# Optimization experiments

Hardware: AMD Instinct MI355X
Metric: run time of the kernel (lower is better)

## Reference

```python
import jax, jax.numpy as jnp
import numpy as np

EPS = 1e-12  # matches torch F.normalize default eps


def setup_inputs() -> dict:
    key = jax.random.key(0)
    img_feats = jax.random.normal(key, (8192, 1024), dtype=jnp.float32)
    return {"img_feats": img_feats}


def reference(img_feats):
    # L2-normalize along feature dim (torch F.normalize: x / max(||x||, eps))
    norm = jnp.maximum(jnp.linalg.norm(img_feats, axis=-1, keepdims=True), EPS)
    feats_n = img_feats / norm                       # [N, D]
    sims = feats_n @ feats_n.T                        # [N, N] cosine similarities
    # mask self-similarity on the diagonal with -inf
    n = sims.shape[0]
    diag = jnp.arange(n)
    sims = sims.at[diag, diag].set(-jnp.inf)
    attn_weights = jax.nn.softmax(sims, axis=-1)      # [N, N]
    out = attn_weights @ img_feats                    # [N, D]
    return out, attn_weights
```

## Files before the change

kernel.cpp:

```cpp
#include <hip/hip_runtime.h>
#include <hip/hip_bf16.h>
#include <stdint.h>

#define NR 8192
#define ND 1024

typedef __attribute__((ext_vector_type(8))) short bf16x8;
typedef __attribute__((ext_vector_type(4))) float f32x4;
typedef __attribute__((ext_vector_type(4))) float fvec4;
typedef __attribute__((ext_vector_type(8))) unsigned short u16x8;

static __device__ __forceinline__ uint16_t f2bf(float f) {
  union { __hip_bfloat16 h; uint16_t u; } cv;
  cv.h = __float2bfloat16(f);
  return cv.u;
}
static __device__ __forceinline__ float bf2f(uint16_t u) {
  union { uint32_t i; float f; } cv;
  cv.i = ((uint32_t)u) << 16;
  return cv.f;
}

__global__ void k_norm(const float* __restrict__ X, uint16_t* __restrict__ Xn) {
  const int row = blockIdx.x;
  const int t = threadIdx.x;
  const float4 v = reinterpret_cast<const float4*>(X + (size_t)row * ND)[t];
  float ss = v.x * v.x + v.y * v.y + v.z * v.z + v.w * v.w;
#pragma unroll
  for (int m = 1; m < 64; m <<= 1) ss += __shfl_xor(ss, m, 64);
  __shared__ float sred[4];
  if ((t & 63) == 0) sred[t >> 6] = ss;
  __syncthreads();
  const float tot = sred[0] + sred[1] + sred[2] + sred[3];
  const float inv = 1.0f / fmaxf(sqrtf(tot), 1e-12f);
  ushort4 o;
  o.x = f2bf(v.x * inv); o.y = f2bf(v.y * inv);
  o.z = f2bf(v.z * inv); o.w = f2bf(v.w * inv);
  reinterpret_cast<ushort4*>(Xn + (size_t)row * ND)[t] = o;
}

__global__ void k_transpose(const float* __restrict__ X, uint16_t* __restrict__ XT) {
  __shared__ uint16_t tile[32][33];
  const int ntr = NR / 32;
  const int bx = blockIdx.x % ntr;
  const int by = blockIdx.x / ntr;
  const int r0 = bx * 32, d0 = by * 32;
  const int t = threadIdx.x;
  const int rr = t >> 3, cc = (t & 7) * 4;
  const float4 v = *reinterpret_cast<const float4*>(&X[(size_t)(r0 + rr) * ND + d0 + cc]);
  tile[cc + 0][rr] = f2bf(v.x);
  tile[cc + 1][rr] = f2bf(v.y);
  tile[cc + 2][rr] = f2bf(v.z);
  tile[cc + 3][rr] = f2bf(v.w);
  __syncthreads();
  ushort4 o;
  o.x = tile[rr][cc + 0]; o.y = tile[rr][cc + 1];
  o.z = tile[rr][cc + 2]; o.w = tile[rr][cc + 3];
  *reinterpret_cast<ushort4*>(&XT[(size_t)(d0 + rr) * NR + r0 + cc]) = o;
}

template <int HALF>
static __device__ __forceinline__ void mfma32(f32x4 (&acc)[8][4],
                                              const bf16x8 (&a_)[4][2],
                                              const bf16x8 (&b_)[4][2]) {
  __builtin_amdgcn_s_setprio(1);
#pragma unroll
  for (int kk = 0; kk < 2; ++kk)
#pragma unroll
    for (int m4 = 0; m4 < 4; ++m4)
#pragma unroll
      for (int n = 0; n < 4; ++n)
        acc[HALF * 4 + m4][n] = __builtin_amdgcn_mfma_f32_16x16x32_bf16(
            a_[m4][kk], b_[n][kk], acc[HALF * 4 + m4][n], 0, 0, 0);
  __builtin_amdgcn_s_setprio(0);
}

#define BAR()    __builtin_amdgcn_s_barrier()
#define LGKM()   asm volatile("s_waitcnt lgkmcnt(0)" ::: "memory")
#define VMW8()   asm volatile("s_waitcnt vmcnt(8)" ::: "memory")
#define VMW0()   asm volatile("s_waitcnt vmcnt(0)" ::: "memory")
#define SCHED0() __builtin_amdgcn_sched_barrier(0)

template <int EPI, int NKT>
static __device__ __forceinline__ void gemm8_core(
    char* sm,
    const uint16_t* __restrict__ A, int lda,
    const uint16_t* __restrict__ B, int ldb,
    int row0, int col0,
    float* __restrict__ C, int ldc,
    uint16_t* __restrict__ Eo, float* __restrict__ partials, int rb, int cb) {
  const int tid = threadIdx.x;
  const int wid = tid >> 6;
  const int lane = tid & 63;
  const int wr = wid >> 2;
  const int wc = wid & 3;
  const int flane = lane & 15;
  const int qw = lane >> 4;
  const int rkey = flane & 7;
  const int rowb = flane * 128;

  const int colb = (((tid & 7) ^ ((tid >> 3) & 7)) * 16);
  const int r0s = tid >> 3;

  const char* const Abyte = (const char*)A + (size_t)row0 * lda * 2;
  const char* const Bbyte = (const char*)B + (size_t)col0 * ldb * 2;

  f32x4 acc[8][4] = {};
  bf16x8 a_[4][2], b_[4][2];

  auto stage = [&](int d, int isB, int h, int t) {
    const char* gb = isB ? Bbyte : Abyte;
    const int ld2 = (isB ? ldb : lda) * 2;
    const char* g0 = gb + (size_t)(h * 128 + r0s) * ld2 + t * 128 + colb;
    const char* g1 = g0 + (size_t)64 * ld2;
    char* l0 = sm + d * 65536 + isB * 32768 + h * 16384 + (wid << 10);
    __builtin_amdgcn_global_load_lds((const __attribute__((address_space(1))) void*)g0,
                                     (__attribute__((address_space(3))) void*)l0, 16, 0, 0);
    __builtin_amdgcn_global_load_lds((const __attribute__((address_space(1))) void*)g1,
                                     (__attribute__((address_space(3))) void*)(l0 + 8192), 16, 0, 0);
  };
  auto stage4 = [&](int d, int t) {
    stage(d, 0, 0, t); stage(d, 0, 1, t); stage(d, 1, 0, t); stage(d, 1, 1, t);
  };
  auto rdA = [&](int d, int mhalf) {
#pragma unroll
    for (int m4 = 0; m4 < 4; ++m4)
#pragma unroll
      for (int kk = 0; kk < 2; ++kk) {
        const int chunk = (qw + kk * 4) ^ rkey;
        a_[m4][kk] = *(const bf16x8*)(sm + d * 65536 + wr * 16384 +
                                      (mhalf * 4 + m4) * 2048 + rowb + chunk * 16);
      }
  };
  auto rdB = [&](int d) {
#pragma unroll
    for (int n = 0; n < 4; ++n)
#pragma unroll
      for (int kk = 0; kk < 2; ++kk) {
        const int chunk = (qw + kk * 4) ^ rkey;
        b_[n][kk] = *(const bf16x8*)(sm + d * 65536 + 32768 + (wc >> 1) * 16384 +
                                     (wc & 1) * 8192 + n * 2048 + rowb + chunk * 16);
      }
  };

  auto ktile = [&](int d) {
    rdB(d); rdA(d, 0);
    LGKM(); SCHED0();
    mfma32<0>(acc, a_, b_);
    rdA(d, 1);
    LGKM(); SCHED0();
    mfma32<1>(acc, a_, b_);
  };

  stage4(0, 0);
  stage4(1, 1);
  VMW8();
  BAR();

  const int niter = NKT / 2;
  for (int i = 0; i < niter; ++i) {
    const int t0 = 2 * i, t1 = t0 + 1;
    ktile(0);
    BAR();
    if (t0 + 2 < NKT) { stage4(0, t0 + 2); VMW8(); }
    else              { VMW0(); }
    BAR();
    ktile(1);
    BAR();
    if (t1 + 2 < NKT) { stage4(1, t1 + 2); VMW8(); }
    else if (t1 + 1 < NKT) { VMW0(); }
    BAR();
  }

  const int e0 = (lane >> 4) * 4;

  if constexpr (EPI == 0) {
    const bool diag = (rb == cb);
    float rp[8][4] = {};
    float rpT[4] = {};
#pragma unroll
    for (int m = 0; m < 8; ++m) {
      const int growb = row0 + wr * 128 + m * 16 + e0;
#pragma unroll
      for (int n = 0; n < 4; ++n) {
        const int gcol = col0 + wc * 64 + n * 16 + flane;
        ushort4 mpack;
#pragma unroll
        for (int e = 0; e < 4; ++e) {
          const int grow = growb + e;
          const float ev = (grow == gcol) ? 0.0f : __expf(acc[m][n][e]);
          const uint16_t eb = f2bf(ev);
          const float evr = bf2f(eb);
          Eo[(size_t)grow * NR + gcol] = eb;
          rp[m][e] += evr;
          rpT[n] += evr;
          ((uint16_t*)&mpack)[e] = eb;
        }
        if (!diag) {
          const int mr = wc * 64 + n * 16 + flane;
          const int mc = wr * 128 + m * 16 + e0;
          int byte = mr * 512 + mc * 2;
          byte ^= (mr & 7) << 4;
          *reinterpret_cast<ushort4*>(sm + byte) = mpack;
        }
      }
    }
#pragma unroll
    for (int msk = 1; msk <= 8; msk <<= 1)
#pragma unroll
      for (int m = 0; m < 8; ++m)
#pragma unroll
        for (int e = 0; e < 4; ++e) rp[m][e] += __shfl_xor(rp[m][e], msk, 64);
#pragma unroll
    for (int msk = 16; msk <= 32; msk <<= 1)
#pragma unroll
      for (int n = 0; n < 4; ++n) rpT[n] += __shfl_xor(rpT[n], msk, 64);

    __syncthreads();
    if (!diag) {
#pragma unroll
      for (int p = 0; p < 16; ++p) {
        const int mr = p * 16 + (tid >> 5);
        const int ch = tid & 31;
        int byte = mr * 512 + ch * 16;
        byte ^= (mr & 7) << 4;
        const u16x8 v = *reinterpret_cast<const u16x8*>(sm + byte);
        *reinterpret_cast<u16x8*>(&Eo[(size_t)(col0 + mr) * NR + row0 + ch * 8]) = v;
      }
    }
    __syncthreads();

    float* sRow = (float*)sm;
    float* sCol = (float*)(sm + 4096);
    if (flane == 0) {
#pragma unroll
      for (int m = 0; m < 8; ++m)
#pragma unroll
        for (int e = 0; e < 4; ++e)
          sRow[wc * 256 + wr * 128 + m * 16 + e0 + e] = rp[m][e];
    }
    if (lane < 16) {
#pragma unroll
      for (int n = 0; n < 4; ++n) sCol[wr * 256 + wc * 64 + n * 16 + lane] = rpT[n];
    }
    __syncthreads();
    if (tid < 256) {
      partials[(size_t)cb * NR + row0 + tid] =
          sRow[tid] + sRow[256 + tid] + sRow[512 + tid] + sRow[768 + tid];
      if (!diag)
        partials[(size_t)rb * NR + col0 + tid] = sCol[tid] + sCol[256 + tid];
    }
  } else {
#pragma unroll
    for (int m = 0; m < 8; ++m)
#pragma unroll
      for (int n = 0; n < 4; ++n)
#pragma unroll
        for (int e = 0; e < 4; ++e)
          C[(size_t)(row0 + wr * 128 + m * 16 + e0 + e) * ldc +
            col0 + wc * 64 + n * 16 + flane] = acc[m][n][e];
  }
}

__global__ __launch_bounds__(512, 2) void k_gemm_sym8(
    const uint16_t* __restrict__ Xn, uint16_t* __restrict__ E,
    float* __restrict__ partials) {
  extern __shared__ char smem[];
  const int nwg = gridDim.x;
  const int cpx = nwg >> 3;
  const int b = blockIdx.x;
  const int swz = (b & 7) * cpx + (b >> 3);
  int rem = swz, rb = 0;
  while (rem >= 32 - rb) { rem -= 32 - rb; ++rb; }
  const int cb = rb + rem;
  gemm8_core<0, 16>(smem, Xn, ND, Xn, ND, rb * 256, cb * 256,
                    nullptr, 0, E, partials, rb, cb);
}

__global__ __launch_bounds__(512, 2) void k_gemm_pv8(
    const uint16_t* __restrict__ E, const uint16_t* __restrict__ XT,
    float* __restrict__ P) {
  extern __shared__ char smem[];
  const int b = blockIdx.x;
  const int swz = (b & 7) * 32 + (b >> 3);
  const int s = swz >> 7;
  const int t = swz & 127;
  const int by = t >> 2, bx = t & 3;
  gemm8_core<1, 64>(smem, E + (size_t)s * 4096, NR, XT + (size_t)s * 4096, NR,
                    by * 256, bx * 256, P + (size_t)s * NR * ND, ND,
                    nullptr, nullptr, 0, 0);
}

__global__ void k_rowsum(const float* __restrict__ partials, float* __restrict__ rowsum,
                         int ncb) {
  const int r = blockIdx.x * blockDim.x + threadIdx.x;
  float s = 0.0f;
  for (int cb = 0; cb < ncb; ++cb) s += partials[(size_t)cb * NR + r];
  rowsum[r] = s;
}

__global__ void k_fixup(const fvec4* __restrict__ P0, const fvec4* __restrict__ P1,
                        const float* __restrict__ rowsum, fvec4* __restrict__ out) {
  const size_t i = (size_t)blockIdx.x * blockDim.x + threadIdx.x;
  const int row = (int)(i >> 8);
  const float inv = 1.0f / rowsum[row];
  const fvec4 a = __builtin_nontemporal_load(&P0[i]);
  const fvec4 b = __builtin_nontemporal_load(&P1[i]);
  const fvec4 o = (a + b) * inv;
  __builtin_nontemporal_store(o, &out[i]);
}

__global__ void k_scale(const uint16_t* __restrict__ E, const float* __restrict__ rowsum,
                        float* __restrict__ attn) {
  const size_t total = (size_t)NR * NR / 8;
  for (size_t i = (size_t)blockIdx.x * blockDim.x + threadIdx.x; i < total;
       i += (size_t)gridDim.x * blockDim.x) {
    const int row = (int)(i >> 10);
    const float inv = 1.0f / rowsum[row];
    const u16x8 e = reinterpret_cast<const u16x8*>(E)[i];
    fvec4 o0, o1;
    o0.x = bf2f(e[0]) * inv; o0.y = bf2f(e[1]) * inv;
    o0.z = bf2f(e[2]) * inv; o0.w = bf2f(e[3]) * inv;
    o1.x = bf2f(e[4]) * inv; o1.y = bf2f(e[5]) * inv;
    o1.z = bf2f(e[6]) * inv; o1.w = bf2f(e[7]) * inv;
    __builtin_nontemporal_store(o0, &reinterpret_cast<fvec4*>(attn)[2 * i + 0]);
    __builtin_nontemporal_store(o1, &reinterpret_cast<fvec4*>(attn)[2 * i + 1]);
  }
}

extern "C" void kernel_launch(void* const* d_in, const int* in_sizes, int n_in,
                              void* d_out, int out_size, void* d_ws, size_t ws_size,
                              hipStream_t stream) {
  const float* X = (const float*)d_in[0];
  float* out = (float*)d_out;
  float* attn = out + (size_t)NR * ND;

  char* ws = (char*)d_ws;
  const size_t off_Xn   = 0;
  const size_t off_XT   = off_Xn + (size_t)NR * ND * 2;
  const size_t off_E    = off_XT + (size_t)ND * NR * 2;
  const size_t off_part = off_E + (size_t)NR * NR * 2;
  const size_t off_rs   = off_part + (size_t)64 * NR * 4;
  const size_t needed   = off_rs + (size_t)NR * 4;
  if (ws_size < needed) return;

  uint16_t* Xn  = (uint16_t*)(ws + off_Xn);
  uint16_t* XT  = (uint16_t*)(ws + off_XT);
  uint16_t* E   = (uint16_t*)(ws + off_E);
  float* partials = (float*)(ws + off_part);
  float* rowsum   = (float*)(ws + off_rs);

  float* P = attn;

  (void)hipFuncSetAttribute((const void*)k_gemm_sym8,
                            hipFuncAttributeMaxDynamicSharedMemorySize, 131072);
  (void)hipFuncSetAttribute((const void*)k_gemm_pv8,
                            hipFuncAttributeMaxDynamicSharedMemorySize, 131072);

  k_norm<<<NR, 256, 0, stream>>>(X, Xn);
  k_transpose<<<(NR / 32) * (ND / 32), 256, 0, stream>>>(X, XT);
  k_gemm_sym8<<<528, 512, 131072, stream>>>(Xn, E, partials);
  k_rowsum<<<NR / 256, 256, 0, stream>>>(partials, rowsum, 32);
  k_gemm_pv8<<<256, 512, 131072, stream>>>(E, XT, P);
  k_fixup<<<NR * ND / 4 / 256, 256, 0, stream>>>(
      (const fvec4*)P, (const fvec4*)(P + (size_t)NR * ND), rowsum, (fvec4*)out);
  k_scale<<<2048, 256, 0, stream>>>(E, rowsum, attn);
}
```

Measured before the change: 373.6 us.

## Interleave half-tile global-to-LDS staging with quarter-tile MFMA phases in GEMM main loop

Result: no change. 377.1 us (+1.0%).

```diff
diff --git a/kernel.cpp b/kernel.cpp
--- a/kernel.cpp
+++ b/kernel.cpp
@@ -59,25 +59,25 @@
   *reinterpret_cast<ushort4*>(&XT[(size_t)(d0 + rr) * NR + r0 + cc]) = o;
 }
 
-template <int HALF>
-static __device__ __forceinline__ void mfma32(f32x4 (&acc)[8][4],
+template <int MH, int NH>
+static __device__ __forceinline__ void mfma16(f32x4 (&acc)[8][4],
                                               const bf16x8 (&a_)[4][2],
-                                              const bf16x8 (&b_)[4][2]) {
+                                              const bf16x8 (&b_)[2][2]) {
   __builtin_amdgcn_s_setprio(1);
 #pragma unroll
   for (int kk = 0; kk < 2; ++kk)
 #pragma unroll
     for (int m4 = 0; m4 < 4; ++m4)
 #pragma unroll
-      for (int n = 0; n < 4; ++n)
-        acc[HALF * 4 + m4][n] = __builtin_amdgcn_mfma_f32_16x16x32_bf16(
-            a_[m4][kk], b_[n][kk], acc[HALF * 4 + m4][n], 0, 0, 0);
+      for (int n2 = 0; n2 < 2; ++n2)
+        acc[MH * 4 + m4][NH * 2 + n2] = __builtin_amdgcn_mfma_f32_16x16x32_bf16(
+            a_[m4][kk], b_[n2][kk], acc[MH * 4 + m4][NH * 2 + n2], 0, 0, 0);
   __builtin_amdgcn_s_setprio(0);
 }
 
 #define BAR()    __builtin_amdgcn_s_barrier()
 #define LGKM()   asm volatile("s_waitcnt lgkmcnt(0)" ::: "memory")
-#define VMW8()   asm volatile("s_waitcnt vmcnt(8)" ::: "memory")
+#define VMW4()   asm volatile("s_waitcnt vmcnt(4)" ::: "memory")
 #define VMW0()   asm volatile("s_waitcnt vmcnt(0)" ::: "memory")
 #define SCHED0() __builtin_amdgcn_sched_barrier(0)
 
@@ -106,9 +106,9 @@
   const char* const Bbyte = (const char*)B + (size_t)col0 * ldb * 2;
 
   f32x4 acc[8][4] = {};
-  bf16x8 a_[4][2], b_[4][2];
-
-  auto stage = [&](int d, int isB, int h, int t) {
+  bf16x8 a_[4][2], b_[2][2];
+
+  auto stageH = [&](int d, int isB, int h, int t) {
     const char* gb = isB ? Bbyte : Abyte;
     const int ld2 = (isB ? ldb : lda) * 2;
     const char* g0 = gb + (size_t)(h * 128 + r0s) * ld2 + t * 128 + colb;
@@ -119,9 +119,6 @@
     __builtin_amdgcn_global_load_lds((const __attribute__((address_space(1))) void*)g1,
                                      (__attribute__((address_space(3))) void*)(l0 + 8192), 16, 0, 0);
   };
-  auto stage4 = [&](int d, int t) {
-    stage(d, 0, 0, t); stage(d, 0, 1, t); stage(d, 1, 0, t); stage(d, 1, 1, t);
-  };
   auto rdA = [&](int d, int mhalf) {
 #pragma unroll
     for (int m4 = 0; m4 < 4; ++m4)
@@ -132,43 +129,50 @@
                                       (mhalf * 4 + m4) * 2048 + rowb + chunk * 16);
       }
   };
-  auto rdB = [&](int d) {
-#pragma unroll
-    for (int n = 0; n < 4; ++n)
+  auto rdB = [&](int d, int nhalf) {
+#pragma unroll
+    for (int n2 = 0; n2 < 2; ++n2)
 #pragma unroll
       for (int kk = 0; kk < 2; ++kk) {
         const int chunk = (qw + kk * 4) ^ rkey;
-        b_[n][kk] = *(const bf16x8*)(sm + d * 65536 + 32768 + (wc >> 1) * 16384 +
-                                     (wc & 1) * 8192 + n * 2048 + rowb + chunk * 16);
+        b_[n2][kk] = *(const bf16x8*)(sm + d * 65536 + 32768 + (wc >> 1) * 16384 +
+                                      (wc & 1) * 8192 + (nhalf * 2 + n2) * 2048 +
+                                      rowb + chunk * 16);
       }
   };
 
-  auto ktile = [&](int d) {
-    rdB(d); rdA(d, 0);
-    LGKM(); SCHED0();
-    mfma32<0>(acc, a_, b_);
-    rdA(d, 1);
-    LGKM(); SCHED0();
-    mfma32<1>(acc, a_, b_);
-  };
-
-  stage4(0, 0);
-  stage4(1, 1);
-  VMW8();
+  stageH(0, 0, 0, 0); stageH(0, 0, 1, 0); stageH(0, 1, 0, 0); stageH(0, 1, 1, 0);
+  stageH(1, 0, 0, 1); stageH(1, 0, 1, 1);
+  VMW4();
   BAR();
 
   const int niter = NKT / 2;
   for (int i = 0; i < niter; ++i) {
     const int t0 = 2 * i, t1 = t0 + 1;
-    ktile(0);
+    const bool s0 = (t0 + 2 < NKT), s1 = (t1 + 2 < NKT);
+    rdA(0, 0); rdB(0, 0);
+    stageH(1, 1, 0, t1); stageH(1, 1, 1, t1);
+    BAR(); LGKM(); SCHED0(); mfma16<0, 0>(acc, a_, b_); BAR();
+    rdB(0, 1);
+    BAR(); LGKM(); SCHED0(); mfma16<0, 1>(acc, a_, b_); BAR();
+    rdA(0, 1);
+    BAR(); LGKM(); SCHED0(); mfma16<1, 1>(acc, a_, b_); BAR();
+    rdB(0, 0);
+    if (s0) { stageH(0, 0, 0, t0 + 2); stageH(0, 0, 1, t0 + 2); }
+    BAR(); LGKM(); SCHED0(); mfma16<1, 0>(acc, a_, b_);
+    if (s0) { VMW4(); } else { VMW0(); }
     BAR();
-    if (t0 + 2 < NKT) { stage4(0, t0 + 2); VMW8(); }
-    else              { VMW0(); }
-    BAR();
-    ktile(1);
-    BAR();
-    if (t1 + 2 < NKT) { stage4(1, t1 + 2); VMW8(); }
-    else if (t1 + 1 < NKT) { VMW0(); }
+    rdA(1, 0); rdB(1, 0);
+    if (s0) { stageH(0, 1, 0, t0 + 2); stageH(0, 1, 1, t0 + 2); }
+    BAR(); LGKM(); SCHED0(); mfma16<0, 0>(acc, a_, b_); BAR();
+    rdB(1, 1);
+    BAR(); LGKM(); SCHED0(); mfma16<0, 1>(acc, a_, b_); BAR();
+    rdA(1, 1);
+    BAR(); LGKM(); SCHED0(); mfma16<1, 1>(acc, a_, b_); BAR();
+    rdB(1, 0);
+    if (s1) { stageH(1, 0, 0, t1 + 2); stageH(1, 0, 1, t1 + 2); }
+    BAR(); LGKM(); SCHED0(); mfma16<1, 0>(acc, a_, b_);
+    if (s1) { VMW4(); } else if (s0) { VMW0(); }
     BAR();
   }
 
```
